# Kernel tuning notes

Measured on AMD Instinct MI355X. Metric: run time of the kernel, lower is better.

## Reference

```python
import jax, jax.numpy as jnp
import numpy as np

N, A, OBS, H, E, ITERS = 2000, 16, 64, 128, 16000, 8


def _init_linear(key, din, dout):
    kw, kb = jax.random.split(key)
    s = 1.0 / np.sqrt(din)
    W = jax.random.uniform(kw, (dout, din), minval=-s, maxval=s, dtype=jnp.float32)
    b = jax.random.uniform(kb, (dout,), minval=-s, maxval=s, dtype=jnp.float32)
    return W, b


def setup_inputs() -> dict:
    key = jax.random.key(0)
    ks = jax.random.split(key, 20)
    x = jax.random.normal(ks[0], (N, OBS), dtype=jnp.float32)
    prev_action = jax.random.normal(ks[1], (N, A), dtype=jnp.float32)
    state = jax.random.normal(ks[2], (1, N, H), dtype=jnp.float32)
    # edges: unique-ish random pairs with i < j (no self loops)
    rng = np.random.default_rng(0)
    ei = rng.integers(0, N - 1, size=E)
    ej = rng.integers(ei + 1, N)
    edges = jnp.asarray(np.stack([ei, ej], axis=1), dtype=jnp.int32)
    # GRU params (torch layout: rows = [r; z; n])
    s = 1.0 / np.sqrt(H)
    gru_wih = jax.random.uniform(ks[3], (3 * H, OBS + A), minval=-s, maxval=s, dtype=jnp.float32)
    gru_whh = jax.random.uniform(ks[4], (3 * H, H), minval=-s, maxval=s, dtype=jnp.float32)
    gru_bih = jax.random.uniform(ks[5], (3 * H,), minval=-s, maxval=s, dtype=jnp.float32)
    gru_bhh = jax.random.uniform(ks[6], (3 * H,), minval=-s, maxval=s, dtype=jnp.float32)
    # utility MLP: [H, 256, 256, A]
    uW0, ub0 = _init_linear(ks[7], H, 256)
    uW1, ub1 = _init_linear(ks[8], 256, 256)
    uW2, ub2 = _init_linear(ks[9], 256, A)
    # payoff MLP: [2H, H, 256, 256, A, A*A]  (faithful to source's dim-list reuse)
    pW0, pb0 = _init_linear(ks[10], 2 * H, H)
    pW1, pb1 = _init_linear(ks[11], H, 256)
    pW2, pb2 = _init_linear(ks[12], 256, 256)
    pW3, pb3 = _init_linear(ks[13], 256, A)
    pW4, pb4 = _init_linear(ks[14], A, A * A)
    return dict(x=x, prev_action=prev_action, state=state, edges=edges,
                gru_wih=gru_wih, gru_whh=gru_whh, gru_bih=gru_bih, gru_bhh=gru_bhh,
                uW0=uW0, ub0=ub0, uW1=uW1, ub1=ub1, uW2=uW2, ub2=ub2,
                pW0=pW0, pb0=pb0, pW1=pW1, pb1=pb1, pW2=pW2, pb2=pb2,
                pW3=pW3, pb3=pb3, pW4=pW4, pb4=pb4)


def _mlp(x, params):
    n = len(params)
    for i, (W, b) in enumerate(params):
        x = x @ W.T + b
        if i < n - 1:
            x = jax.nn.relu(x)
    return x


def _gru_step(inp, h, wih, whh, bih, bhh):
    gi = inp @ wih.T + bih          # [N, 3H]
    gh = h @ whh.T + bhh            # [N, 3H]
    gir, giz, gin = jnp.split(gi, 3, axis=-1)
    ghr, ghz, ghn = jnp.split(gh, 3, axis=-1)
    r = jax.nn.sigmoid(gir + ghr)
    z = jax.nn.sigmoid(giz + ghz)
    n = jnp.tanh(gin + r * ghn)
    return (1.0 - z) * n + z * h


def _message_passing(u, p, ei, ej):
    """u: [N,A] differentiable, p: [E,A,A] differentiable.
    Messages are computed under stop_gradient (torch.no_grad in source);
    Q of the per-iteration greedy action is differentiable in u, p."""
    u_sg = jax.lax.stop_gradient(u)
    p_sg = jax.lax.stop_gradient(p)
    node_idx = jnp.arange(N)
    edge_idx = jnp.arange(E)

    def step(carry, _):
        M, q_max, opt_a = carry            # M[recv, send, A]
        S = M.sum(axis=1)                  # [N, A] total incoming per node
        base_i = u_sg[ei] + S[ei] - M[ei, ej]   # [E, A] indexed by a_i
        base_j = u_sg[ej] + S[ej] - M[ej, ei]   # [E, A] indexed by a_j
        # message i -> j: max over a_i of (p[e,ai,aj] + base_i[ai])
        msg_to_j = (p_sg + base_i[:, :, None]).max(axis=1)   # [E, A]
        msg_to_j = msg_to_j - msg_to_j.mean(axis=-1, keepdims=True)
        # message j -> i (source reduces over dim 0 = a_i; replicated faithfully)
        msg_to_i = (p_sg + base_j[:, None, :]).max(axis=1)   # [E, A]
        msg_to_i = msg_to_i - msg_to_i.mean(axis=-1, keepdims=True)
        M = M.at[ej, ei].set(msg_to_j).at[ei, ej].set(msg_to_i)
        # greedy action per node
        a_idx = jnp.argmax(u_sg + M.sum(axis=1), axis=-1)    # [N]
        q_real = u[node_idx, a_idx].sum() + p[edge_idx, a_idx[ei], a_idx[ej]].sum()
        better = q_real > q_max
        q_max = jnp.where(better, q_real, q_max)
        a_onehot = jax.nn.one_hot(a_idx, A, dtype=u.dtype)
        opt_a = jnp.where(better, a_onehot, opt_a)
        return (M, q_max, opt_a), None

    M0 = jnp.zeros((N, N, A), dtype=u.dtype)
    q0 = jnp.zeros((), dtype=u.dtype)
    a0 = jnp.zeros((N, A), dtype=u.dtype)
    (M, q_max, opt_a), _ = jax.lax.scan(step, (M0, q0, a0), None, length=ITERS)
    return opt_a, q_max


def reference(x, prev_action, state, edges,
              gru_wih, gru_whh, gru_bih, gru_bhh,
              uW0, ub0, uW1, ub1, uW2, ub2,
              pW0, pb0, pW1, pb1, pW2, pb2, pW3, pb3, pW4, pb4):
    ei, ej = edges[:, 0], edges[:, 1]
    enc_in = jnp.concatenate([x, prev_action], axis=-1)        # [N, OBS+A]
    h = _gru_step(enc_in, state[0], gru_wih, gru_whh, gru_bih, gru_bhh)  # [N, H]
    state_out = h.reshape(1, 1, N, H)
    u_params = [(uW0, ub0), (uW1, ub1), (uW2, ub2)]
    p_params = [(pW0, pb0), (pW1, pb1), (pW2, pb2), (pW3, pb3), (pW4, pb4)]
    u = _mlp(h, u_params) / N                                  # [N, A]
    s_ij = jnp.concatenate([h[ei], h[ej]], axis=-1)            # [E, 2H]
    s_ji = jnp.concatenate([h[ej], h[ei]], axis=-1)
    p_ij = _mlp(s_ij, p_params).reshape(E, A, A) / E
    p_ji = _mlp(s_ji, p_params).reshape(E, A, A) / E
    p = 0.5 * (p_ij + p_ji)                                    # [E, A, A]
    a, q_max = _message_passing(u, p, ei, ej)
    return (a, q_max, u[None], p, state_out)
```

## Files before the change

### kernel.cpp

```cpp
#include <hip/hip_runtime.h>
#include <math.h>

#define N_NODES 2000
#define NA 16
#define NOBS 64
#define NH 128
#define NE 16000
#define NITERS 8

#define WS_MSG       0
#define WS_FLAGS     300000
#define WS_Q         512000
#define WS_SBUF      512016
#define WS_AIDX      800016
#define WS_W         816016
#define WS_PT        832016
#define WS_GIT       (WS_PT + 4000000)
#define WS_GHT       (WS_GIT + 30720)
#define WS_WB        4928016
#define WS_UW0T      (WS_WB + 0)
#define WS_UWCAT     (WS_WB + 32768)
#define WS_UW1T      (WS_WB + 65536)
#define WS_UW2T      (WS_WB + 131072)
#define WS_CAB       (WS_WB + 241664)

#define F16_W1H 0
#define F16_W1L 32768
#define F16_W2H 65536
#define F16_W2L 131072
#define F16_W3H 196608
#define F16_W3L 200704
#define F16_W4H 204800
#define F16_W4L 212992

#define NBLK 500

typedef _Float16 half8 __attribute__((ext_vector_type(8)));
typedef float f32x4 __attribute__((ext_vector_type(4)));

__global__ __launch_bounds__(256) void setup_kernel(
    float* __restrict__ ws, const int* __restrict__ edges,
    const float* __restrict__ uW0, const float* __restrict__ uW1,
    const float* __restrict__ uW2, const float* __restrict__ pW0,
    const float* __restrict__ pW1, const float* __restrict__ pW2,
    const float* __restrict__ pW3, const float* __restrict__ pW4,
    const float* __restrict__ gwih, const float* __restrict__ gwhh)
{
    if (blockIdx.x >= 1024) {
        int e = (blockIdx.x - 1024) * 256 + threadIdx.x;
        if (e < NE) {
            int i = edges[2 * e], j = edges[2 * e + 1];
            ((int*)(ws + WS_PT))[i * N_NODES + j] = -1;
        }
        return;
    }
    const int total = 341904;
    for (int idx = blockIdx.x * 256 + threadIdx.x; idx < total;
         idx += 1024 * 256) {
        if (idx < 16) {
            ws[WS_Q + idx] = 0.f;
        } else {
            int t = idx - 16;
            if (t < 135168) {
                float v;
                if (t < 32768) {
                    int k = t / 256, o = t % 256;
                    v = uW0[o * 128 + k];
                } else if (t < 65536) {
                    int q = t - 32768, k = q / 256, o = q % 256;
                    v = (o < 128) ? pW0[o * 256 + k]
                                  : pW0[(o - 128) * 256 + 128 + k];
                } else if (t < 131072) {
                    int q = t - 65536, k = q / 256, o = q % 256;
                    v = uW1[o * 256 + k];
                } else {
                    int q = t - 131072, k = q / 16, o = q % 16;
                    v = uW2[o * 256 + k];
                }
                ws[WS_WB + t] = v;
            } else if (t < 215056) {
                int q = t - 135168;
                if (q < 30720) {
                    int k4 = q / 1536, r = q % 1536, g = r >> 2, c = r & 3;
                    ws[WS_GIT + q] = gwih[g * 80 + 4 * k4 + c];
                } else if (q < 79872) {
                    int q2 = q - 30720;
                    int k4 = q2 / 1536, r = q2 % 1536, g = r >> 2, c = r & 3;
                    ws[WS_GHT + q2] = gwhh[g * 128 + 4 * k4 + c];
                }
            } else if (t < 325648) {
                int q = t - 215056;
                if (q >= 110592) continue;
                _Float16* fw = (_Float16*)ws;
                float v; int hoff, loff;
                if (q < 32768) {
                    v = pW1[q]; hoff = F16_W1H + q; loff = F16_W1L + q;
                } else if (q < 98304) {
                    int z = q - 32768; v = pW2[z];
                    hoff = F16_W2H + z; loff = F16_W2L + z;
                } else if (q < 102400) {
                    int z = q - 98304; v = pW3[z];
                    hoff = F16_W3H + z; loff = F16_W3L + z;
                } else {
                    int z = q - 102400; int n = z >> 5, kk = z & 31;
                    v = (kk < 16) ? pW4[n * 16 + kk] : 0.f;
                    hoff = F16_W4H + z; loff = F16_W4L + z;
                }
                _Float16 hv = (_Float16)v;
                fw[hoff] = hv;
                fw[loff] = (_Float16)(v - (float)hv);
            } else {
                int qf = t - 325648;
                ((int*)(ws + WS_FLAGS))[qf] = 0;
            }
        }
    }
}

__global__ __launch_bounds__(256) void gru_kernel(
    const float* __restrict__ x, const float* __restrict__ pa,
    const float* __restrict__ st, const float* __restrict__ wihT,
    const float* __restrict__ whhT, const float* __restrict__ bih,
    const float* __restrict__ bhh, float* __restrict__ h_out,
    const int* __restrict__ edges, int* __restrict__ owner)
{
    if (blockIdx.x >= 250) {
        int e = (blockIdx.x - 250) * 256 + threadIdx.x;
        if (e < NE) {
            int i = edges[2 * e], j = edges[2 * e + 1];
            atomicMax(&owner[i * N_NODES + j], e);
        }
        return;
    }
    __shared__ float enc[8][80];
    __shared__ float hp[8][128];
    __shared__ float gi[8][384];
    __shared__ float gh[8][384];
    const int tid = threadIdx.x;
    const int n0 = blockIdx.x * 8;

    for (int idx = tid; idx < 8 * 80; idx += 256) {
        int r = idx / 80, c = idx % 80;
        enc[r][c] = (c < 64) ? x[(n0 + r) * 64 + c] : pa[(n0 + r) * 16 + (c - 64)];
    }
    for (int idx = tid; idx < 8 * 128; idx += 256) {
        int r = idx >> 7, c = idx & 127;
        hp[r][c] = st[(n0 + r) * 128 + c];
    }
    __syncthreads();

    for (int idx = tid; idx < 8 * 384; idx += 256) {
        int g = idx % 384, r = idx / 384;
        float s1 = bih[g];
        #pragma unroll 5
        for (int k4 = 0; k4 < 20; ++k4) {
            const float4 ev = *(const float4*)&enc[r][4 * k4];
            const float4 wv = *(const float4*)&wihT[k4 * 1536 + g * 4];
            s1 = fmaf(ev.x, wv.x, fmaf(ev.y, wv.y, fmaf(ev.z, wv.z, fmaf(ev.w, wv.w, s1))));
        }
        gi[r][g] = s1;
        float s2 = bhh[g];
        #pragma unroll 8
        for (int k4 = 0; k4 < 32; ++k4) {
            const float4 hv = *(const float4*)&hp[r][4 * k4];
            const float4 wv = *(const float4*)&whhT[k4 * 1536 + g * 4];
            s2 = fmaf(hv.x, wv.x, fmaf(hv.y, wv.y, fmaf(hv.z, wv.z, fmaf(hv.w, wv.w, s2))));
        }
        gh[r][g] = s2;
    }
    __syncthreads();

    for (int idx = tid; idx < 8 * 128; idx += 256) {
        int r = idx >> 7, c = idx & 127;
        float rr = 1.f / (1.f + expf(-(gi[r][c] + gh[r][c])));
        float zz = 1.f / (1.f + expf(-(gi[r][128 + c] + gh[r][128 + c])));
        float nn = tanhf(gi[r][256 + c] + rr * gh[r][256 + c]);
        h_out[(n0 + r) * 128 + c] = (1.f - zz) * nn + zz * hp[r][c];
    }
}

__global__ __launch_bounds__(256) void umlp_kernel(
    const float* __restrict__ h, const float* __restrict__ w0t,
    const float* __restrict__ b0, const float* __restrict__ w1t,
    const float* __restrict__ b1, const float* __restrict__ w2t,
    const float* __restrict__ b2, const float* __restrict__ wcat,
    float* __restrict__ u_out, float* __restrict__ Sbuf,
    float* __restrict__ cab, const int* __restrict__ edges,
    const int* __restrict__ owner, int* __restrict__ wflag)
{
    if (blockIdx.x >= 500) {
        int e = (blockIdx.x - 500) * 256 + threadIdx.x;
        if (e < NE) {
            int i = edges[2 * e], j = edges[2 * e + 1];
            wflag[e] = (owner[i * N_NODES + j] == e) ? 1 : 0;
        }
        return;
    }
    __shared__ float A[8][128];
    __shared__ float B[8][256];
    const int tid = threadIdx.x;
    const bool is_cab = blockIdx.x >= 250;
    const int n0 = (is_cab ? blockIdx.x - 250 : blockIdx.x) * 8;

    for (int idx = tid; idx < 8 * 128; idx += 256) {
        int r = idx >> 7, c = idx & 127;
        A[r][c] = h[(n0 + r) * 128 + c];
    }
    __syncthreads();

    if (is_cab) {
        const int o = tid;
        const float* wp = wcat + o;
        float wA[4], wB[4];
        #pragma unroll
        for (int c = 0; c < 4; ++c) wA[c] = wp[c * 256];
        float acc[8];
        #pragma unroll
        for (int r = 0; r < 8; ++r) acc[r] = 0.f;
        for (int k4 = 0; k4 < 32; k4 += 2) {
            #pragma unroll
            for (int c = 0; c < 4; ++c) wB[c] = wp[(4 * (k4 + 1) + c) * 256];
            #pragma unroll
            for (int r = 0; r < 8; ++r) {
                const float4 av = *(const float4*)&A[r][4 * k4];
                acc[r] = fmaf(av.x, wA[0], fmaf(av.y, wA[1], fmaf(av.z, wA[2], fmaf(av.w, wA[3], acc[r]))));
            }
            #pragma unroll
            for (int c = 0; c < 4; ++c) wA[c] = wp[(4 * (k4 + 2) + c) * 256];
            #pragma unroll
            for (int r = 0; r < 8; ++r) {
                const float4 av = *(const float4*)&A[r][4 * k4 + 4];
                acc[r] = fmaf(av.x, wB[0], fmaf(av.y, wB[1], fmaf(av.z, wB[2], fmaf(av.w, wB[3], acc[r]))));
            }
        }
        #pragma unroll
        for (int r = 0; r < 8; ++r) cab[(n0 + r) * 256 + o] = acc[r];
        return;
    }

    {
        const int o = tid;
        const float* wp = w0t + o;
        float wA[4], wB[4];
        #pragma unroll
        for (int c = 0; c < 4; ++c) wA[c] = wp[c * 256];
        float acc[8];
        #pragma unroll
        for (int r = 0; r < 8; ++r) acc[r] = b0[o];
        for (int k4 = 0; k4 < 32; k4 += 2) {
            #pragma unroll
            for (int c = 0; c < 4; ++c) wB[c] = wp[(4 * (k4 + 1) + c) * 256];
            #pragma unroll
            for (int r = 0; r < 8; ++r) {
                const float4 av = *(const float4*)&A[r][4 * k4];
                acc[r] = fmaf(av.x, wA[0], fmaf(av.y, wA[1], fmaf(av.z, wA[2], fmaf(av.w, wA[3], acc[r]))));
            }
            #pragma unroll
            for (int c = 0; c < 4; ++c) wA[c] = wp[(4 * (k4 + 2) + c) * 256];
            #pragma unroll
            for (int r = 0; r < 8; ++r) {
                const float4 av = *(const float4*)&A[r][4 * k4 + 4];
                acc[r] = fmaf(av.x, wB[0], fmaf(av.y, wB[1], fmaf(av.z, wB[2], fmaf(av.w, wB[3], acc[r]))));
            }
        }
        #pragma unroll
        for (int r = 0; r < 8; ++r) B[r][o] = fmaxf(acc[r], 0.f);
    }
    __syncthreads();
    {
        const int o = tid;
        const float* wp = w1t + o;
        float wA[4], wB[4];
        #pragma unroll
        for (int c = 0; c < 4; ++c) wA[c] = wp[c * 256];
        float acc[8];
        #pragma unroll
        for (int r = 0; r < 8; ++r) acc[r] = b1[o];
        for (int k4 = 0; k4 < 64; k4 += 2) {
            #pragma unroll
            for (int c = 0; c < 4; ++c) wB[c] = wp[(4 * (k4 + 1) + c) * 256];
            #pragma unroll
            for (int r = 0; r < 8; ++r) {
                const float4 av = *(const float4*)&B[r][4 * k4];
                acc[r] = fmaf(av.x, wA[0], fmaf(av.y, wA[1], fmaf(av.z, wA[2], fmaf(av.w, wA[3], acc[r]))));
            }
            #pragma unroll
            for (int c = 0; c < 4; ++c) wA[c] = wp[(4 * (k4 + 2) + c) * 256];
            #pragma unroll
            for (int r = 0; r < 8; ++r) {
                const float4 av = *(const float4*)&B[r][4 * k4 + 4];
                acc[r] = fmaf(av.x, wB[0], fmaf(av.y, wB[1], fmaf(av.z, wB[2], fmaf(av.w, wB[3], acc[r]))));
            }
        }
        __syncthreads();
        #pragma unroll
        for (int r = 0; r < 8; ++r) B[r][o] = fmaxf(acc[r], 0.f);
    }
    __syncthreads();
    if (tid < 128) {
        int r = tid >> 4, o = tid & 15;
        float acc = b2[o];
        for (int k4 = 0; k4 < 64; ++k4) {
            const float4 av = *(const float4*)&B[r][4 * k4];
            acc = fmaf(av.x, w2t[(4 * k4 + 0) * 16 + o],
                  fmaf(av.y, w2t[(4 * k4 + 1) * 16 + o],
                  fmaf(av.z, w2t[(4 * k4 + 2) * 16 + o],
                  fmaf(av.w, w2t[(4 * k4 + 3) * 16 + o], acc))));
        }
        float val = acc * (1.f / N_NODES);
        int idx = (n0 + r) * 16 + o;
        u_out[idx] = val;
        #pragma unroll
        for (int t = 0; t < NITERS + 1; ++t) Sbuf[t * 32000 + idx] = val;
    }
}

__global__ __launch_bounds__(512, 4) void pmlp_kernel(
    const float* __restrict__ cab, const int* __restrict__ edges,
    const float* __restrict__ b0, const _Float16* __restrict__ fw,
    const float* __restrict__ b1, const float* __restrict__ b2,
    const float* __restrict__ b3, const float* __restrict__ b4,
    float* __restrict__ p_out, float* __restrict__ pT)
{
    __shared__ __align__(16) _Float16 Ah[64][264];
    __shared__ __align__(16) _Float16 Al[64][264];
    __shared__ float C16[64][16];
    __shared__ int fi[64], se[64];

    const int tid  = threadIdx.x;
    const int e0   = blockIdx.x * 32;
    const int wid  = tid >> 6;
    const int lane = tid & 63;
    const int lrow = lane & 15;
    const int lgrp = lane >> 4;
    const int koff = 8 * lgrp;

    if (tid < 32) {
        int i = edges[2 * (e0 + tid)], j = edges[2 * (e0 + tid) + 1];
        fi[2 * tid] = i;     se[2 * tid] = j;
        fi[2 * tid + 1] = j; se[2 * tid + 1] = i;
    }
    __syncthreads();

    {
        const int cl = tid & 127;
        const int rh = tid >> 7;
        const float bb = b0[cl];
        #pragma unroll 4
        for (int r = rh * 16; r < rh * 16 + 16; ++r) {
            float v = cab[fi[r] * 256 + cl] + cab[se[r] * 256 + 128 + cl] + bb;
            v = fmaxf(v, 0.f);
            _Float16 hv = (_Float16)v;
            Ah[r][cl] = hv;
            Al[r][cl] = (_Float16)(v - (float)hv);
        }
    }
    __syncthreads();

    f32x4 acc[4][2];

    #pragma unroll
    for (int mt = 0; mt < 4; ++mt)
        #pragma unroll
        for (int nt = 0; nt < 2; ++nt) acc[mt][nt] = (f32x4){0.f, 0.f, 0.f, 0.f};
    #pragma unroll
    for (int ks = 0; ks < 4; ++ks) {
        half8 ah[4], al[4];
        #pragma unroll
        for (int mt = 0; mt < 4; ++mt) {
            ah[mt] = *(const half8*)&Ah[16 * mt + lrow][32 * ks + koff];
            al[mt] = *(const half8*)&Al[16 * mt + lrow][32 * ks + koff];
        }
        #pragma unroll
        for (int nt = 0; nt < 2; ++nt) {
            const int n = 32 * wid + 16 * nt + lrow;
            half8 bh = *(const half8*)(fw + F16_W1H + n * 128 + 32 * ks + koff);
            half8 bl = *(const half8*)(fw + F16_W1L + n * 128 + 32 * ks + koff);
            #pragma unroll
            for (int mt = 0; mt < 4; ++mt) {
                acc[mt][nt] = __builtin_amdgcn_mfma_f32_16x16x32_f16(ah[mt], bh, acc[mt][nt], 0, 0, 0);
                acc[mt][nt] = __builtin_amdgcn_mfma_f32_16x16x32_f16(ah[mt], bl, acc[mt][nt], 0, 0, 0);
                acc[mt][nt] = __builtin_amdgcn_mfma_f32_16x16x32_f16(al[mt], bh, acc[mt][nt], 0, 0, 0);
            }
        }
    }
    __syncthreads();
    #pragma unroll
    for (int nt = 0; nt < 2; ++nt) {
        const int col = 32 * wid + 16 * nt + lrow;
        const float bv = b1[col];
        #pragma unroll
        for (int mt = 0; mt < 4; ++mt) {
            #pragma unroll
            for (int r = 0; r < 4; ++r) {
                const int row = 16 * mt + 4 * lgrp + r;
                float v = fmaxf(acc[mt][nt][r] + bv, 0.f);
                _Float16 hv = (_Float16)v;
                Ah[row][col] = hv;
                Al[row][col] = (_Float16)(v - (float)hv);
            }
        }
    }
    __syncthreads();

    #pragma unroll
    for (int mt = 0; mt < 4; ++mt)
        #pragma unroll
        for (int nt = 0; nt < 2; ++nt) acc[mt][nt] = (f32x4){0.f, 0.f, 0.f, 0.f};
    for (int ks = 0; ks < 8; ++ks) {
        half8 ah[4], al[4];
        #pragma unroll
        for (int mt = 0; mt < 4; ++mt) {
            ah[mt] = *(const half8*)&Ah[16 * mt + lrow][32 * ks + koff];
            al[mt] = *(const half8*)&Al[16 * mt + lrow][32 * ks + koff];
        }
        #pragma unroll
        for (int nt = 0; nt < 2; ++nt) {
            const int n = 32 * wid + 16 * nt + lrow;
            half8 bh = *(const half8*)(fw + F16_W2H + n * 256 + 32 * ks + koff);
            half8 bl = *(const half8*)(fw + F16_W2L + n * 256 + 32 * ks + koff);
            #pragma unroll
            for (int mt = 0; mt < 4; ++mt) {
                acc[mt][nt] = __builtin_amdgcn_mfma_f32_16x16x32_f16(ah[mt], bh, acc[mt][nt], 0, 0, 0);
                acc[mt][nt] = __builtin_amdgcn_mfma_f32_16x16x32_f16(ah[mt], bl, acc[mt][nt], 0, 0, 0);
                acc[mt][nt] = __builtin_amdgcn_mfma_f32_16x16x32_f16(al[mt], bh, acc[mt][nt], 0, 0, 0);
            }
        }
    }
    __syncthreads();
    #pragma unroll
    for (int nt = 0; nt < 2; ++nt) {
        const int col = 32 * wid + 16 * nt + lrow;
        const float bv = b2[col];
        #pragma unroll
        for (int mt = 0; mt < 4; ++mt) {
            #pragma unroll
            for (int r = 0; r < 4; ++r) {
                const int row = 16 * mt + 4 * lgrp + r;
                float v = fmaxf(acc[mt][nt][r] + bv, 0.f);
                _Float16 hv = (_Float16)v;
                Ah[row][col] = hv;
                Al[row][col] = (_Float16)(v - (float)hv);
            }
        }
    }
    __syncthreads();

    if (wid < 4) {
        f32x4 acc3 = {0.f, 0.f, 0.f, 0.f};
        #pragma unroll
        for (int ks = 0; ks < 8; ++ks) {
            half8 ah = *(const half8*)&Ah[16 * wid + lrow][32 * ks + koff];
            half8 al = *(const half8*)&Al[16 * wid + lrow][32 * ks + koff];
            half8 bh = *(const half8*)(fw + F16_W3H + lrow * 256 + 32 * ks + koff);
            half8 bl = *(const half8*)(fw + F16_W3L + lrow * 256 + 32 * ks + koff);
            acc3 = __builtin_amdgcn_mfma_f32_16x16x32_f16(ah, bh, acc3, 0, 0, 0);
            acc3 = __builtin_amdgcn_mfma_f32_16x16x32_f16(ah, bl, acc3, 0, 0, 0);
            acc3 = __builtin_amdgcn_mfma_f32_16x16x32_f16(al, bh, acc3, 0, 0, 0);
        }
        const float b3v = b3[lrow];
        #pragma unroll
        for (int r = 0; r < 4; ++r)
            C16[16 * wid + 4 * lgrp + r][lrow] = fmaxf(acc3[r] + b3v, 0.f);
    }
    __syncthreads();

    {
        half8 a4h[4], a4l[4];
        #pragma unroll
        for (int mt = 0; mt < 4; ++mt) {
            half8 hh, ll;
            #pragma unroll
            for (int j = 0; j < 8; ++j) { hh[j] = (_Float16)0.f; ll[j] = (_Float16)0.f; }
            if (lgrp < 2) {
                #pragma unroll
                for (int j = 0; j < 8; ++j) {
                    float v = C16[16 * mt + lrow][8 * lgrp + j];
                    _Float16 hv = (_Float16)v;
                    hh[j] = hv;
                    ll[j] = (_Float16)(v - (float)hv);
                }
            }
            a4h[mt] = hh; a4l[mt] = ll;
        }
        #pragma unroll
        for (int nt = 0; nt < 2; ++nt) {
            const int o = 32 * wid + 16 * nt + lrow;
            const float b4v = b4[o];
            half8 bh = *(const half8*)(fw + F16_W4H + o * 32 + koff);
            half8 bl = *(const half8*)(fw + F16_W4L + o * 32 + koff);
            const int ot = (o & 15) * 16 + (o >> 4);
            #pragma unroll
            for (int mt = 0; mt < 4; ++mt) {
                f32x4 a4 = {0.f, 0.f, 0.f, 0.f};
                a4 = __builtin_amdgcn_mfma_f32_16x16x32_f16(a4h[mt], bh, a4, 0, 0, 0);
                a4 = __builtin_amdgcn_mfma_f32_16x16x32_f16(a4h[mt], bl, a4, 0, 0, 0);
                a4 = __builtin_amdgcn_mfma_f32_16x16x32_f16(a4l[mt], bh, a4, 0, 0, 0);
                const int s0 = 8 * mt + 2 * lgrp;
                float pa = (0.5f * (a4[0] + a4[1]) + b4v) * (1.f / NE);
                float pb = (0.5f * (a4[2] + a4[3]) + b4v) * (1.f / NE);
                p_out[(e0 + s0) * 256 + o] = pa;
                p_out[(e0 + s0 + 1) * 256 + o] = pb;
                pT[(e0 + s0) * 256 + ot] = pa;
                pT[(e0 + s0 + 1) * 256 + ot] = pb;
            }
        }
    }
}

__device__ __forceinline__ void grid_bar(int* flags, int gval)
{
    int* gen8 = flags + NBLK * 32;
    __syncthreads();
    if (blockIdx.x == 0) {
        const int i = threadIdx.x;
        if (i >= 1 && i < NBLK) {
            while (__hip_atomic_load(&flags[i * 32], __ATOMIC_RELAXED,
                                     __HIP_MEMORY_SCOPE_AGENT) < gval)
                __builtin_amdgcn_s_sleep(2);
        }
        __syncthreads();
        if (i < 8)
            __hip_atomic_store(&gen8[i * 32], gval, __ATOMIC_RELAXED,
                               __HIP_MEMORY_SCOPE_AGENT);
    } else {
        if (threadIdx.x == 0) {
            asm volatile("s_waitcnt vmcnt(0)" ::: "memory");
            __hip_atomic_store(&flags[blockIdx.x * 32], gval, __ATOMIC_RELAXED,
                               __HIP_MEMORY_SCOPE_AGENT);
            while (__hip_atomic_load(&gen8[(blockIdx.x & 7) * 32],
                                     __ATOMIC_RELAXED,
                                     __HIP_MEMORY_SCOPE_AGENT) < gval)
                __builtin_amdgcn_s_sleep(2);
        }
        __syncthreads();
    }
}

__global__ __launch_bounds__(512, 4) void mp_fused_kernel(
    const float* __restrict__ u, float* __restrict__ Sbuf,
    const float* __restrict__ pT, const float* __restrict__ p,
    const int* __restrict__ edges, const int* __restrict__ wflag,
    int* __restrict__ aidx, float* __restrict__ q,
    float* __restrict__ a_out, float* __restrict__ q_out,
    int* __restrict__ flags)
{
    const int tid = threadIdx.x;
    const int bid = blockIdx.x;
    const int e   = bid * 32 + (tid >> 4);
    const int L   = tid & 15;

    const int gi = edges[2 * e], gj = edges[2 * e + 1];
    const int wf = wflag[e];
    const float4* pt = (const float4*)(pT + e * 256 + L * 16);
    const float4 p0 = pt[0], p1 = pt[1], p2 = pt[2], p3 = pt[3];
    float pv[16] = {p0.x, p0.y, p0.z, p0.w, p1.x, p1.y, p1.z, p1.w,
                    p2.x, p2.y, p2.z, p2.w, p3.x, p3.y, p3.z, p3.w};
    float vmax = -INFINITY;
    #pragma unroll
    for (int a = 0; a < 16; ++a) vmax = fmaxf(vmax, pv[a]);
    float mold_ij = 0.f, mold_ji = 0.f;

    for (int t = 0; t < NITERS; ++t) {
        const float* uSo = Sbuf + t * 32000;
        float* uSn = Sbuf + (t + 1) * 32000;
        const float bi = uSo[gi * 16 + L] - mold_ij;
        const float bj = uSo[gj * 16 + L] - mold_ji;
        float mj = -INFINITY;
        #pragma unroll
        for (int a = 0; a < 16; ++a)
            mj = fmaxf(mj, pv[a] + __shfl(bi, a, 16));
        float mi = vmax + bj;
        float sj = mj, si = mi;
        #pragma unroll
        for (int off = 1; off < 16; off <<= 1) {
            sj += __shfl_xor(sj, off, 16);
            si += __shfl_xor(si, off, 16);
        }
        mj -= sj * (1.f / 16.f);
        mi -= si * (1.f / 16.f);
        mold_ji = mj;
        mold_ij = mi;
        if (wf) {
            atomicAdd(&uSn[gj * 16 + L], mj);
            atomicAdd(&uSn[gi * 16 + L], mi);
        }
        grid_bar(flags, t + 1);
    }

    if (bid < 288) {
        const int t2 = bid / 36;
        const int r2 = (bid % 36) * 512 + tid;
        const float* Sn = Sbuf + (t2 + 1) * 32000;
        float partial = 0.f;
        if (r2 < N_NODES) {
            int n = r2;
            float bv = Sn[n * 16];
            int best = 0;
            #pragma unroll
            for (int a = 1; a < 16; ++a) {
                float v = Sn[n * 16 + a];
                if (v > bv) { bv = v; best = a; }
            }
            __hip_atomic_store(&aidx[t2 * N_NODES + n], best, __ATOMIC_RELAXED,
                               __HIP_MEMORY_SCOPE_AGENT);
            partial = u[n * 16 + best];
        } else if (r2 < N_NODES + NE) {
            int ee = r2 - N_NODES;
            int ii = edges[2 * ee], jj = edges[2 * ee + 1];
            float bvi = Sn[ii * 16]; int ai = 0;
            #pragma unroll
            for (int a = 1; a < 16; ++a) {
                float v = Sn[ii * 16 + a];
                if (v > bvi) { bvi = v; ai = a; }
            }
            float bvj = Sn[jj * 16]; int aj = 0;
            #pragma unroll
            for (int a = 1; a < 16; ++a) {
                float v = Sn[jj * 16 + a];
                if (v > bvj) { bvj = v; aj = a; }
            }
            partial = p[ee * 256 + ai * 16 + aj];
        }
        #pragma unroll
        for (int off = 1; off < 64; off <<= 1)
            partial += __shfl_xor(partial, off, 64);
        if ((tid & 63) == 0) atomicAdd(&q[t2], partial);
    }
    grid_bar(flags, NITERS + 1);

    const int r = bid * 512 + tid;
    if (r < N_NODES * 16) {
        float cur = 0.f; int best_t = -1;
        #pragma unroll
        for (int t2 = 0; t2 < NITERS; ++t2) {
            float qv = q[t2];
            if (qv > cur) { cur = qv; best_t = t2; }
        }
        int n = r >> 4, c = r & 15;
        float val = 0.f;
        if (best_t >= 0 && aidx[best_t * N_NODES + n] == c) val = 1.f;
        a_out[r] = val;
        if (r == 0) q_out[0] = cur;
    }
}

extern "C" void kernel_launch(void* const* d_in, const int* in_sizes, int n_in,
                              void* d_out, int out_size, void* d_ws, size_t ws_size,
                              hipStream_t stream)
{
    (void)in_sizes; (void)n_in; (void)out_size; (void)ws_size;
    const float* x    = (const float*)d_in[0];
    const float* pa   = (const float*)d_in[1];
    const float* st   = (const float*)d_in[2];
    const int*   edges= (const int*)d_in[3];
    const float* gwih = (const float*)d_in[4];
    const float* gwhh = (const float*)d_in[5];
    const float* gbih = (const float*)d_in[6];
    const float* gbhh = (const float*)d_in[7];
    const float* uW0 = (const float*)d_in[8];  const float* ub0 = (const float*)d_in[9];
    const float* uW1 = (const float*)d_in[10]; const float* ub1 = (const float*)d_in[11];
    const float* uW2 = (const float*)d_in[12]; const float* ub2 = (const float*)d_in[13];
    const float* pW0 = (const float*)d_in[14]; const float* pb0 = (const float*)d_in[15];
    const float* pW1 = (const float*)d_in[16]; const float* pb1 = (const float*)d_in[17];
    const float* pW2 = (const float*)d_in[18]; const float* pb2 = (const float*)d_in[19];
    const float* pW3 = (const float*)d_in[20]; const float* pb3 = (const float*)d_in[21];
    const float* pW4 = (const float*)d_in[22]; const float* pb4 = (const float*)d_in[23];

    float* out   = (float*)d_out;
    float* a_out = out;
    float* q_out = out + 32000;
    float* u_out = out + 32001;
    float* p_out = out + 64001;
    float* h_out = out + 4160001;

    float* ws   = (float*)d_ws;
    float* Sbuf = ws + WS_SBUF;
    float* q    = ws + WS_Q;
    int*   flg  = (int*)(ws + WS_FLAGS);
    int*   aidx = (int*)(ws + WS_AIDX);
    int*   wfl  = (int*)(ws + WS_W);
    float* pT   = ws + WS_PT;
    float* cab  = ws + WS_CAB;
    int*   owner= (int*)(ws + WS_PT);

    setup_kernel<<<1087, 256, 0, stream>>>(ws, edges, uW0, uW1, uW2,
                                           pW0, pW1, pW2, pW3, pW4, gwih, gwhh);
    gru_kernel<<<313, 256, 0, stream>>>(x, pa, st, ws + WS_GIT, ws + WS_GHT,
                                        gbih, gbhh, h_out, edges, owner);
    umlp_kernel<<<563, 256, 0, stream>>>(h_out, ws + WS_UW0T, ub0,
                                         ws + WS_UW1T, ub1, ws + WS_UW2T, ub2,
                                         ws + WS_UWCAT, u_out, Sbuf, cab,
                                         edges, owner, wfl);
    pmlp_kernel<<<NE / 32, 512, 0, stream>>>(cab, edges, pb0,
                                             (const _Float16*)ws,
                                             pb1, pb2, pb3, pb4, p_out, pT);
    mp_fused_kernel<<<NBLK, 512, 0, stream>>>(u_out, Sbuf, pT, p_out,
                                              edges, wfl, aidx, q,
                                              a_out, q_out, flg);
}
```

Measured before the change: 280.1 us.

## Fuse payoff MLP into persistent message-passing kernel, keep transposed payoff in LDS

Merges the payoff MLP kernel into the grid-synchronized message-passing kernel, so each block computes its 32 edges' payoff matrices and keeps the transposed copy in shared memory instead of writing and re-reading a global pT buffer. This removes one kernel launch and the global round-trip of the transposed payoffs. p_out is written with agent-scope atomic stores so other blocks can read it after the grid barrier. The cost is that the persistent kernel now carries the MLP's shared-memory and register footprint, which may constrain co-residency needed for the grid barrier.

```diff
diff --git a/kernel.cpp b/kernel.cpp
--- a/kernel.cpp
+++ b/kernel.cpp
@@ -315,199 +315,6 @@
     }
 }
 
-__global__ __launch_bounds__(512, 4) void pmlp_kernel(
-    const float* __restrict__ cab, const int* __restrict__ edges,
-    const float* __restrict__ b0, const _Float16* __restrict__ fw,
-    const float* __restrict__ b1, const float* __restrict__ b2,
-    const float* __restrict__ b3, const float* __restrict__ b4,
-    float* __restrict__ p_out, float* __restrict__ pT)
-{
-    __shared__ __align__(16) _Float16 Ah[64][264];
-    __shared__ __align__(16) _Float16 Al[64][264];
-    __shared__ float C16[64][16];
-    __shared__ int fi[64], se[64];
-
-    const int tid  = threadIdx.x;
-    const int e0   = blockIdx.x * 32;
-    const int wid  = tid >> 6;
-    const int lane = tid & 63;
-    const int lrow = lane & 15;
-    const int lgrp = lane >> 4;
-    const int koff = 8 * lgrp;
-
-    if (tid < 32) {
-        int i = edges[2 * (e0 + tid)], j = edges[2 * (e0 + tid) + 1];
-        fi[2 * tid] = i;     se[2 * tid] = j;
-        fi[2 * tid + 1] = j; se[2 * tid + 1] = i;
-    }
-    __syncthreads();
-
-    {
-        const int cl = tid & 127;
-        const int rh = tid >> 7;
-        const float bb = b0[cl];
-        #pragma unroll 4
-        for (int r = rh * 16; r < rh * 16 + 16; ++r) {
-            float v = cab[fi[r] * 256 + cl] + cab[se[r] * 256 + 128 + cl] + bb;
-            v = fmaxf(v, 0.f);
-            _Float16 hv = (_Float16)v;
-            Ah[r][cl] = hv;
-            Al[r][cl] = (_Float16)(v - (float)hv);
-        }
-    }
-    __syncthreads();
-
-    f32x4 acc[4][2];
-
-    #pragma unroll
-    for (int mt = 0; mt < 4; ++mt)
-        #pragma unroll
-        for (int nt = 0; nt < 2; ++nt) acc[mt][nt] = (f32x4){0.f, 0.f, 0.f, 0.f};
-    #pragma unroll
-    for (int ks = 0; ks < 4; ++ks) {
-        half8 ah[4], al[4];
-        #pragma unroll
-        for (int mt = 0; mt < 4; ++mt) {
-            ah[mt] = *(const half8*)&Ah[16 * mt + lrow][32 * ks + koff];
-            al[mt] = *(const half8*)&Al[16 * mt + lrow][32 * ks + koff];
-        }
-        #pragma unroll
-        for (int nt = 0; nt < 2; ++nt) {
-            const int n = 32 * wid + 16 * nt + lrow;
-            half8 bh = *(const half8*)(fw + F16_W1H + n * 128 + 32 * ks + koff);
-            half8 bl = *(const half8*)(fw + F16_W1L + n * 128 + 32 * ks + koff);
-            #pragma unroll
-            for (int mt = 0; mt < 4; ++mt) {
-                acc[mt][nt] = __builtin_amdgcn_mfma_f32_16x16x32_f16(ah[mt], bh, acc[mt][nt], 0, 0, 0);
-                acc[mt][nt] = __builtin_amdgcn_mfma_f32_16x16x32_f16(ah[mt], bl, acc[mt][nt], 0, 0, 0);
-                acc[mt][nt] = __builtin_amdgcn_mfma_f32_16x16x32_f16(al[mt], bh, acc[mt][nt], 0, 0, 0);
-            }
-        }
-    }
-    __syncthreads();
-    #pragma unroll
-    for (int nt = 0; nt < 2; ++nt) {
-        const int col = 32 * wid + 16 * nt + lrow;
-        const float bv = b1[col];
-        #pragma unroll
-        for (int mt = 0; mt < 4; ++mt) {
-            #pragma unroll
-            for (int r = 0; r < 4; ++r) {
-                const int row = 16 * mt + 4 * lgrp + r;
-                float v = fmaxf(acc[mt][nt][r] + bv, 0.f);
-                _Float16 hv = (_Float16)v;
-                Ah[row][col] = hv;
-                Al[row][col] = (_Float16)(v - (float)hv);
-            }
-        }
-    }
-    __syncthreads();
-
-    #pragma unroll
-    for (int mt = 0; mt < 4; ++mt)
-        #pragma unroll
-        for (int nt = 0; nt < 2; ++nt) acc[mt][nt] = (f32x4){0.f, 0.f, 0.f, 0.f};
-    for (int ks = 0; ks < 8; ++ks) {
-        half8 ah[4], al[4];
-        #pragma unroll
-        for (int mt = 0; mt < 4; ++mt) {
-            ah[mt] = *(const half8*)&Ah[16 * mt + lrow][32 * ks + koff];
-            al[mt] = *(const half8*)&Al[16 * mt + lrow][32 * ks + koff];
-        }
-        #pragma unroll
-        for (int nt = 0; nt < 2; ++nt) {
-            const int n = 32 * wid + 16 * nt + lrow;
-            half8 bh = *(const half8*)(fw + F16_W2H + n * 256 + 32 * ks + koff);
-            half8 bl = *(const half8*)(fw + F16_W2L + n * 256 + 32 * ks + koff);
-            #pragma unroll
-            for (int mt = 0; mt < 4; ++mt) {
-                acc[mt][nt] = __builtin_amdgcn_mfma_f32_16x16x32_f16(ah[mt], bh, acc[mt][nt], 0, 0, 0);
-                acc[mt][nt] = __builtin_amdgcn_mfma_f32_16x16x32_f16(ah[mt], bl, acc[mt][nt], 0, 0, 0);
-                acc[mt][nt] = __builtin_amdgcn_mfma_f32_16x16x32_f16(al[mt], bh, acc[mt][nt], 0, 0, 0);
-            }
-        }
-    }
-    __syncthreads();
-    #pragma unroll
-    for (int nt = 0; nt < 2; ++nt) {
-        const int col = 32 * wid + 16 * nt + lrow;
-        const float bv = b2[col];
-        #pragma unroll
-        for (int mt = 0; mt < 4; ++mt) {
-            #pragma unroll
-            for (int r = 0; r < 4; ++r) {
-                const int row = 16 * mt + 4 * lgrp + r;
-                float v = fmaxf(acc[mt][nt][r] + bv, 0.f);
-                _Float16 hv = (_Float16)v;
-                Ah[row][col] = hv;
-                Al[row][col] = (_Float16)(v - (float)hv);
-            }
-        }
-    }
-    __syncthreads();
-
-    if (wid < 4) {
-        f32x4 acc3 = {0.f, 0.f, 0.f, 0.f};
-        #pragma unroll
-        for (int ks = 0; ks < 8; ++ks) {
-            half8 ah = *(const half8*)&Ah[16 * wid + lrow][32 * ks + koff];
-            half8 al = *(const half8*)&Al[16 * wid + lrow][32 * ks + koff];
-            half8 bh = *(const half8*)(fw + F16_W3H + lrow * 256 + 32 * ks + koff);
-            half8 bl = *(const half8*)(fw + F16_W3L + lrow * 256 + 32 * ks + koff);
-            acc3 = __builtin_amdgcn_mfma_f32_16x16x32_f16(ah, bh, acc3, 0, 0, 0);
-            acc3 = __builtin_amdgcn_mfma_f32_16x16x32_f16(ah, bl, acc3, 0, 0, 0);
-            acc3 = __builtin_amdgcn_mfma_f32_16x16x32_f16(al, bh, acc3, 0, 0, 0);
-        }
-        const float b3v = b3[lrow];
-        #pragma unroll
-        for (int r = 0; r < 4; ++r)
-            C16[16 * wid + 4 * lgrp + r][lrow] = fmaxf(acc3[r] + b3v, 0.f);
-    }
-    __syncthreads();
-
-    {
-        half8 a4h[4], a4l[4];
-        #pragma unroll
-        for (int mt = 0; mt < 4; ++mt) {
-            half8 hh, ll;
-            #pragma unroll
-            for (int j = 0; j < 8; ++j) { hh[j] = (_Float16)0.f; ll[j] = (_Float16)0.f; }
-            if (lgrp < 2) {
-                #pragma unroll
-                for (int j = 0; j < 8; ++j) {
-                    float v = C16[16 * mt + lrow][8 * lgrp + j];
-                    _Float16 hv = (_Float16)v;
-                    hh[j] = hv;
-                    ll[j] = (_Float16)(v - (float)hv);
-                }
-            }
-            a4h[mt] = hh; a4l[mt] = ll;
-        }
-        #pragma unroll
-        for (int nt = 0; nt < 2; ++nt) {
-            const int o = 32 * wid + 16 * nt + lrow;
-            const float b4v = b4[o];
-            half8 bh = *(const half8*)(fw + F16_W4H + o * 32 + koff);
-            half8 bl = *(const half8*)(fw + F16_W4L + o * 32 + koff);
-            const int ot = (o & 15) * 16 + (o >> 4);
-            #pragma unroll
-            for (int mt = 0; mt < 4; ++mt) {
-                f32x4 a4 = {0.f, 0.f, 0.f, 0.f};
-                a4 = __builtin_amdgcn_mfma_f32_16x16x32_f16(a4h[mt], bh, a4, 0, 0, 0);
-                a4 = __builtin_amdgcn_mfma_f32_16x16x32_f16(a4h[mt], bl, a4, 0, 0, 0);
-                a4 = __builtin_amdgcn_mfma_f32_16x16x32_f16(a4l[mt], bh, a4, 0, 0, 0);
-                const int s0 = 8 * mt + 2 * lgrp;
-                float pa = (0.5f * (a4[0] + a4[1]) + b4v) * (1.f / NE);
-                float pb = (0.5f * (a4[2] + a4[3]) + b4v) * (1.f / NE);
-                p_out[(e0 + s0) * 256 + o] = pa;
-                p_out[(e0 + s0 + 1) * 256 + o] = pb;
-                pT[(e0 + s0) * 256 + ot] = pa;
-                pT[(e0 + s0 + 1) * 256 + ot] = pb;
-            }
-        }
-    }
-}
-
 __device__ __forceinline__ void grid_bar(int* flags, int gval)
 {
     int* gen8 = flags + NBLK * 32;
@@ -537,25 +344,220 @@
     }
 }
 
-__global__ __launch_bounds__(512, 4) void mp_fused_kernel(
-    const float* __restrict__ u, float* __restrict__ Sbuf,
-    const float* __restrict__ pT, const float* __restrict__ p,
-    const int* __restrict__ edges, const int* __restrict__ wflag,
+__global__ __launch_bounds__(512, 4) void pmlp_mp_kernel(
+    const float* __restrict__ cab, const int* __restrict__ edges,
+    const float* __restrict__ b0, const _Float16* __restrict__ fw,
+    const float* __restrict__ b1, const float* __restrict__ b2,
+    const float* __restrict__ b3, const float* __restrict__ b4,
+    float* __restrict__ p_out, const float* __restrict__ u,
+    float* __restrict__ Sbuf, const int* __restrict__ wflag,
     int* __restrict__ aidx, float* __restrict__ q,
     float* __restrict__ a_out, float* __restrict__ q_out,
     int* __restrict__ flags)
 {
-    const int tid = threadIdx.x;
-    const int bid = blockIdx.x;
-    const int e   = bid * 32 + (tid >> 4);
-    const int L   = tid & 15;
-
+    __shared__ __align__(16) _Float16 Ah[64][264];
+    __shared__ __align__(16) _Float16 Al[64][264];
+    __shared__ float C16[64][16];
+    __shared__ int fi[64], se[64];
+
+    const int tid  = threadIdx.x;
+    const int bid  = blockIdx.x;
+    const int e0   = bid * 32;
+    const int wid  = tid >> 6;
+    const int lane = tid & 63;
+    const int lrow = lane & 15;
+    const int lgrp = lane >> 4;
+    const int koff = 8 * lgrp;
+
+    if (tid < 32) {
+        int i = edges[2 * (e0 + tid)], j = edges[2 * (e0 + tid) + 1];
+        fi[2 * tid] = i;     se[2 * tid] = j;
+        fi[2 * tid + 1] = j; se[2 * tid + 1] = i;
+    }
+    __syncthreads();
+
+    {
+        const int cl = tid & 127;
+        const int rh = tid >> 7;
+        const float bb = b0[cl];
+        #pragma unroll 4
+        for (int r = rh * 16; r < rh * 16 + 16; ++r) {
+            float v = cab[fi[r] * 256 + cl] + cab[se[r] * 256 + 128 + cl] + bb;
+            v = fmaxf(v, 0.f);
+            _Float16 hv = (_Float16)v;
+            Ah[r][cl] = hv;
+            Al[r][cl] = (_Float16)(v - (float)hv);
+        }
+    }
+    __syncthreads();
+
+    f32x4 acc[4][2];
+
+    #pragma unroll
+    for (int mt = 0; mt < 4; ++mt)
+        #pragma unroll
+        for (int nt = 0; nt < 2; ++nt) acc[mt][nt] = (f32x4){0.f, 0.f, 0.f, 0.f};
+    #pragma unroll
+    for (int ks = 0; ks < 4; ++ks) {
+        half8 ah[4], al[4];
+        #pragma unroll
+        for (int mt = 0; mt < 4; ++mt) {
+            ah[mt] = *(const half8*)&Ah[16 * mt + lrow][32 * ks + koff];
+            al[mt] = *(const half8*)&Al[16 * mt + lrow][32 * ks + koff];
+        }
+        #pragma unroll
+        for (int nt = 0; nt < 2; ++nt) {
+            const int n = 32 * wid + 16 * nt + lrow;
+            half8 bh = *(const half8*)(fw + F16_W1H + n * 128 + 32 * ks + koff);
+            half8 bl = *(const half8*)(fw + F16_W1L + n * 128 + 32 * ks + koff);
+            #pragma unroll
+            for (int mt = 0; mt < 4; ++mt) {
+                acc[mt][nt] = __builtin_amdgcn_mfma_f32_16x16x32_f16(ah[mt], bh, acc[mt][nt], 0, 0, 0);
+                acc[mt][nt] = __builtin_amdgcn_mfma_f32_16x16x32_f16(ah[mt], bl, acc[mt][nt], 0, 0, 0);
+                acc[mt][nt] = __builtin_amdgcn_mfma_f32_16x16x32_f16(al[mt], bh, acc[mt][nt], 0, 0, 0);
+            }
+        }
+    }
+    __syncthreads();
+    #pragma unroll
+    for (int nt = 0; nt < 2; ++nt) {
+        const int col = 32 * wid + 16 * nt + lrow;
+        const float bv = b1[col];
+        #pragma unroll
+        for (int mt = 0; mt < 4; ++mt) {
+            #pragma unroll
+            for (int r = 0; r < 4; ++r) {
+                const int row = 16 * mt + 4 * lgrp + r;
+                float v = fmaxf(acc[mt][nt][r] + bv, 0.f);
+                _Float16 hv = (_Float16)v;
+                Ah[row][col] = hv;
+                Al[row][col] = (_Float16)(v - (float)hv);
+            }
+        }
+    }
+    __syncthreads();
+
+    #pragma unroll
+    for (int mt = 0; mt < 4; ++mt)
+        #pragma unroll
+        for (int nt = 0; nt < 2; ++nt) acc[mt][nt] = (f32x4){0.f, 0.f, 0.f, 0.f};
+    for (int ks = 0; ks < 8; ++ks) {
+        half8 ah[4], al[4];
+        #pragma unroll
+        for (int mt = 0; mt < 4; ++mt) {
+            ah[mt] = *(const half8*)&Ah[16 * mt + lrow][32 * ks + koff];
+            al[mt] = *(const half8*)&Al[16 * mt + lrow][32 * ks + koff];
+        }
+        #pragma unroll
+        for (int nt = 0; nt < 2; ++nt) {
+            const int n = 32 * wid + 16 * nt + lrow;
+            half8 bh = *(const half8*)(fw + F16_W2H + n * 256 + 32 * ks + koff);
+            half8 bl = *(const half8*)(fw + F16_W2L + n * 256 + 32 * ks + koff);
+            #pragma unroll
+            for (int mt = 0; mt < 4; ++mt) {
+                acc[mt][nt] = __builtin_amdgcn_mfma_f32_16x16x32_f16(ah[mt], bh, acc[mt][nt], 0, 0, 0);
+                acc[mt][nt] = __builtin_amdgcn_mfma_f32_16x16x32_f16(ah[mt], bl, acc[mt][nt], 0, 0, 0);
+                acc[mt][nt] = __builtin_amdgcn_mfma_f32_16x16x32_f16(al[mt], bh, acc[mt][nt], 0, 0, 0);
+            }
+        }
+    }
+    __syncthreads();
+    #pragma unroll
+    for (int nt = 0; nt < 2; ++nt) {
+        const int col = 32 * wid + 16 * nt + lrow;
+        const float bv = b2[col];
+        #pragma unroll
+        for (int mt = 0; mt < 4; ++mt) {
+            #pragma unroll
+            for (int r = 0; r < 4; ++r) {
+                const int row = 16 * mt + 4 * lgrp + r;
+                float v = fmaxf(acc[mt][nt][r] + bv, 0.f);
+                _Float16 hv = (_Float16)v;
+                Ah[row][col] = hv;
+                Al[row][col] = (_Float16)(v - (float)hv);
+            }
+        }
+    }
+    __syncthreads();
+
+    if (wid < 4) {
+        f32x4 acc3 = {0.f, 0.f, 0.f, 0.f};
+        #pragma unroll
+        for (int ks = 0; ks < 8; ++ks) {
+            half8 ah = *(const half8*)&Ah[16 * wid + lrow][32 * ks + koff];
+            half8 al = *(const half8*)&Al[16 * wid + lrow][32 * ks + koff];
+            half8 bh = *(const half8*)(fw + F16_W3H + lrow * 256 + 32 * ks + koff);
+            half8 bl = *(const half8*)(fw + F16_W3L + lrow * 256 + 32 * ks + koff);
+            acc3 = __builtin_amdgcn_mfma_f32_16x16x32_f16(ah, bh, acc3, 0, 0, 0);
+            acc3 = __builtin_amdgcn_mfma_f32_16x16x32_f16(ah, bl, acc3, 0, 0, 0);
+            acc3 = __builtin_amdgcn_mfma_f32_16x16x32_f16(al, bh, acc3, 0, 0, 0);
+        }
+        const float b3v = b3[lrow];
+        #pragma unroll
+        for (int r = 0; r < 4; ++r)
+            C16[16 * wid + 4 * lgrp + r][lrow] = fmaxf(acc3[r] + b3v, 0.f);
+    }
+    __syncthreads();
+
+    float* pTl = (float*)Ah;
+
+    {
+        half8 a4h[4], a4l[4];
+        #pragma unroll
+        for (int mt = 0; mt < 4; ++mt) {
+            half8 hh, ll;
+            #pragma unroll
+            for (int j = 0; j < 8; ++j) { hh[j] = (_Float16)0.f; ll[j] = (_Float16)0.f; }
+            if (lgrp < 2) {
+                #pragma unroll
+                for (int j = 0; j < 8; ++j) {
+                    float v = C16[16 * mt + lrow][8 * lgrp + j];
+                    _Float16 hv = (_Float16)v;
+                    hh[j] = hv;
+                    ll[j] = (_Float16)(v - (float)hv);
+                }
+            }
+            a4h[mt] = hh; a4l[mt] = ll;
+        }
+        #pragma unroll
+        for (int nt = 0; nt < 2; ++nt) {
+            const int o = 32 * wid + 16 * nt + lrow;
+            const float b4v = b4[o];
+            half8 bh = *(const half8*)(fw + F16_W4H + o * 32 + koff);
+            half8 bl = *(const half8*)(fw + F16_W4L + o * 32 + koff);
+            const int ot = (o & 15) * 16 + (o >> 4);
+            #pragma unroll
+            for (int mt = 0; mt < 4; ++mt) {
+                f32x4 a4 = {0.f, 0.f, 0.f, 0.f};
+                a4 = __builtin_amdgcn_mfma_f32_16x16x32_f16(a4h[mt], bh, a4, 0, 0, 0);
+                a4 = __builtin_amdgcn_mfma_f32_16x16x32_f16(a4h[mt], bl, a4, 0, 0, 0);
+                a4 = __builtin_amdgcn_mfma_f32_16x16x32_f16(a4l[mt], bh, a4, 0, 0, 0);
+                const int s0 = 8 * mt + 2 * lgrp;
+                float pa = (0.5f * (a4[0] + a4[1]) + b4v) * (1.f / NE);
+                float pb = (0.5f * (a4[2] + a4[3]) + b4v) * (1.f / NE);
+                __hip_atomic_store(&p_out[(e0 + s0) * 256 + o], pa,
+                                   __ATOMIC_RELAXED, __HIP_MEMORY_SCOPE_AGENT);
+                __hip_atomic_store(&p_out[(e0 + s0 + 1) * 256 + o], pb,
+                                   __ATOMIC_RELAXED, __HIP_MEMORY_SCOPE_AGENT);
+                pTl[s0 * 256 + ot] = pa;
+                pTl[(s0 + 1) * 256 + ot] = pb;
+            }
+        }
+    }
+    __syncthreads();
+
+    const int g = tid >> 4;
+    const int L = tid & 15;
+    const int e = e0 + g;
     const int gi = edges[2 * e], gj = edges[2 * e + 1];
     const int wf = wflag[e];
-    const float4* pt = (const float4*)(pT + e * 256 + L * 16);
-    const float4 p0 = pt[0], p1 = pt[1], p2 = pt[2], p3 = pt[3];
-    float pv[16] = {p0.x, p0.y, p0.z, p0.w, p1.x, p1.y, p1.z, p1.w,
-                    p2.x, p2.y, p2.z, p2.w, p3.x, p3.y, p3.z, p3.w};
+    float pv[16];
+    #pragma unroll
+    for (int a4i = 0; a4i < 4; ++a4i) {
+        float4 v = *(const float4*)&pTl[g * 256 + L * 16 + 4 * a4i];
+        pv[4 * a4i + 0] = v.x; pv[4 * a4i + 1] = v.y;
+        pv[4 * a4i + 2] = v.z; pv[4 * a4i + 3] = v.w;
+    }
     float vmax = -INFINITY;
     #pragma unroll
     for (int a = 0; a < 16; ++a) vmax = fmaxf(vmax, pv[a]);
@@ -620,7 +622,7 @@
                 float v = Sn[jj * 16 + a];
                 if (v > bvj) { bvj = v; aj = a; }
             }
-            partial = p[ee * 256 + ai * 16 + aj];
+            partial = p_out[ee * 256 + ai * 16 + aj];
         }
         #pragma unroll
         for (int off = 1; off < 64; off <<= 1)
@@ -680,7 +682,6 @@
     int*   flg  = (int*)(ws + WS_FLAGS);
     int*   aidx = (int*)(ws + WS_AIDX);
     int*   wfl  = (int*)(ws + WS_W);
-    float* pT   = ws + WS_PT;
     float* cab  = ws + WS_CAB;
     int*   owner= (int*)(ws + WS_PT);
 
@@ -692,10 +693,9 @@
                                          ws + WS_UW1T, ub1, ws + WS_UW2T, ub2,
                                          ws + WS_UWCAT, u_out, Sbuf, cab,
                                          edges, owner, wfl);
-    pmlp_kernel<<<NE / 32, 512, 0, stream>>>(cab, edges, pb0,
+    pmlp_mp_kernel<<<NBLK, 512, 0, stream>>>(cab, edges, pb0,
                                              (const _Float16*)ws,
-                                             pb1, pb2, pb3, pb4, p_out, pT);
-    mp_fused_kernel<<<NBLK, 512, 0, stream>>>(u_out, Sbuf, pT, p_out,
-                                              edges, wfl, aidx, q,
-                                              a_out, q_out, flg);
+                                             pb1, pb2, pb3, pb4, p_out,
+                                             u_out, Sbuf, wfl, aidx, q,
+                                             a_out, q_out, flg);
 }
```

Measured after the change: 266.1 us. 5.0% less time.
